# Kernel tuning notes

Measured on AMD Instinct MI355X. Metric: run time of the kernel, lower is better.

The kernel has to match this reference:

```python
import jax, jax.numpy as jnp
import numpy as np

N_NODES = 50000
N_EDGES = 800000
DIM = 64
N_HEADS = 4


def setup_inputs() -> dict:
    key = jax.random.key(0)
    ks = jax.random.split(key, 7)
    x = jax.random.normal(ks[0], (N_NODES, DIM), dtype=jnp.float32)
    Wq = jax.random.normal(ks[1], (DIM, DIM), dtype=jnp.float32) / np.sqrt(DIM)
    Wk = jax.random.normal(ks[2], (DIM, DIM), dtype=jnp.float32) / np.sqrt(DIM)
    Wv = jax.random.normal(ks[3], (DIM, DIM), dtype=jnp.float32) / np.sqrt(DIM)
    Wo = jax.random.normal(ks[4], (DIM, DIM), dtype=jnp.float32) / np.sqrt(DIM)
    src = jax.random.randint(ks[5], (N_EDGES,), 0, N_NODES, dtype=jnp.int32)
    dst = jax.random.randint(ks[6], (N_EDGES,), 0, N_NODES, dtype=jnp.int32)
    return {"x": x, "Wq": Wq, "Wk": Wk, "Wv": Wv, "Wo": Wo, "src": src, "dst": dst}


def _scatter_softmax(scores, dst, n_nodes):
    # scores: [E, H]; per-destination-node softmax over incoming edges.
    m = jax.ops.segment_max(scores, dst, num_segments=n_nodes)  # [N, H]
    m = jnp.maximum(m, jnp.float32(-1e9))  # mirror the -1e9 init of the torch code
    ex = jnp.exp(scores - m[dst])  # [E, H]
    denom = jax.ops.segment_sum(ex, dst, num_segments=n_nodes)  # [N, H]
    return ex / (denom[dst] + 1e-9)


def reference(x, Wq, Wk, Wv, Wo, src, dst):
    N, D = x.shape
    H = N_HEADS
    Dh = D // H
    q = (x @ Wq).reshape(N, H, Dh)
    k = (x @ Wk).reshape(N, H, Dh)
    v = (x @ Wv).reshape(N, H, Dh)
    # per-edge attention logits: [E, H]
    scores = jnp.einsum("ehd,ehd->eh", q[dst], k[src]) / jnp.sqrt(jnp.float32(Dh))
    alpha = _scatter_softmax(scores, dst, N)  # [E, H]
    # weighted aggregation of source values onto destination nodes
    agg = jax.ops.segment_sum(alpha[:, :, None] * v[src], dst, num_segments=N)  # [N, H, Dh]
    return agg.reshape(N, D) @ Wo
```

## Files before the change

### kernel.cpp

```cpp
#include <hip/hip_runtime.h>
#include <math.h>

#define HEADS 4
#define DH 16
#define D 64
#define MAXDEG 64
#define NXCD 8

typedef unsigned short ushort_t;
typedef unsigned int uint_t;

__device__ __forceinline__ float bf2f(ushort_t u) {
    return __uint_as_float(((uint_t)u) << 16);
}
__device__ __forceinline__ ushort_t f2bf(float f) {
    uint_t u = __float_as_uint(f);
    u = (u + 0x7FFFu + ((u >> 16) & 1u)) >> 16;
    return (ushort_t)u;
}
__device__ __forceinline__ float bflo(uint_t u) { return __uint_as_float(u << 16); }
__device__ __forceinline__ float bfhi(uint_t u) { return __uint_as_float(u & 0xFFFF0000u); }
__device__ __forceinline__ uint_t pack2(float a, float b) {
    return (uint_t)f2bf(a) | ((uint_t)f2bf(b) << 16);
}

__global__ __launch_bounds__(256) void qkv_kernel(const float* __restrict__ x,
                                                  const float* __restrict__ Wq,
                                                  const float* __restrict__ Wk,
                                                  const float* __restrict__ Wv,
                                                  ushort_t* __restrict__ qbf,
                                                  ushort_t* __restrict__ kbf,
                                                  ushort_t* __restrict__ vbf,
                                                  int* __restrict__ cursor,
                                                  int N) {
    __shared__ float wq[D][D];
    __shared__ float wk[D][D];
    __shared__ float wv[D][D];
    __shared__ float xs[16][D];

    int tid = threadIdx.x;
    for (int i = tid; i < D * D; i += 256) {
        wq[i >> 6][i & 63] = Wq[i];
        wk[i >> 6][i & 63] = Wk[i];
        wv[i >> 6][i & 63] = Wv[i];
    }

    int c = tid & 63;
    int g = tid >> 6;
    int row = tid >> 4;
    int col4 = tid & 15;

    int ntiles = (N + 15) >> 4;
    for (int tile = blockIdx.x; tile < ntiles; tile += gridDim.x) {
        int n0t = tile * 16;
        __syncthreads();
        float4 xv = make_float4(0.f, 0.f, 0.f, 0.f);
        if (n0t + row < N) xv = *(const float4*)(x + (size_t)(n0t + row) * D + col4 * 4);
        *(float4*)&xs[row][col4 * 4] = xv;
        __syncthreads();

        float aq0=0,aq1=0,aq2=0,aq3=0, ak0=0,ak1=0,ak2=0,ak3=0, av0=0,av1=0,av2=0,av3=0;
#pragma unroll 8
        for (int d = 0; d < D; ++d) {
            float wqv = wq[d][c], wkv = wk[d][c], wvv = wv[d][c];
            float x0 = xs[g*4+0][d], x1 = xs[g*4+1][d], x2 = xs[g*4+2][d], x3 = xs[g*4+3][d];
            aq0 += x0*wqv; ak0 += x0*wkv; av0 += x0*wvv;
            aq1 += x1*wqv; ak1 += x1*wkv; av1 += x1*wvv;
            aq2 += x2*wqv; ak2 += x2*wkv; av2 += x2*wvv;
            aq3 += x3*wqv; ak3 += x3*wkv; av3 += x3*wvv;
        }
        int nb = n0t + g * 4;
        if (nb+0 < N) { qbf[(size_t)(nb+0)*D+c]=f2bf(aq0); kbf[(size_t)(nb+0)*D+c]=f2bf(ak0); vbf[(size_t)(nb+0)*D+c]=f2bf(av0); }
        if (nb+1 < N) { qbf[(size_t)(nb+1)*D+c]=f2bf(aq1); kbf[(size_t)(nb+1)*D+c]=f2bf(ak1); vbf[(size_t)(nb+1)*D+c]=f2bf(av1); }
        if (nb+2 < N) { qbf[(size_t)(nb+2)*D+c]=f2bf(aq2); kbf[(size_t)(nb+2)*D+c]=f2bf(ak2); vbf[(size_t)(nb+2)*D+c]=f2bf(av2); }
        if (nb+3 < N) { qbf[(size_t)(nb+3)*D+c]=f2bf(aq3); kbf[(size_t)(nb+3)*D+c]=f2bf(ak3); vbf[(size_t)(nb+3)*D+c]=f2bf(av3); }
    }

    for (int i = blockIdx.x * 256 + tid; i < N; i += gridDim.x * 256) cursor[i] = 0;
}

__global__ __launch_bounds__(256) void scatter_kernel(const int* __restrict__ src,
                                                      const int* __restrict__ dst,
                                                      int* __restrict__ cursor,
                                                      ushort_t* __restrict__ csr,
                                                      int E, int N) {
    int p      = blockIdx.x & (NXCD - 1);
    int chunk  = blockIdx.x >> 3;
    int nchunk = gridDim.x >> 3;
    int lo = (int)((long long)N * p / NXCD);
    int hi = (int)((long long)N * (p + 1) / NXCD);
    int e0 = (int)((long long)E * chunk / nchunk);
    int e1 = (int)((long long)E * (chunk + 1) / nchunk);

    for (int e = e0 + threadIdx.x; e < e1; e += 256) {
        int d = dst[e];
        if (d >= lo && d < hi) {
            int pos = atomicAdd(&cursor[d], 1);
            if (pos < MAXDEG) csr[(size_t)d * MAXDEG + pos] = (ushort_t)src[e];
        }
    }
}

__global__ __launch_bounds__(256) void attn_kernel(const ushort_t* __restrict__ qbf,
                                                   const ushort_t* __restrict__ kbf,
                                                   const ushort_t* __restrict__ vbf,
                                                   const ushort_t* __restrict__ csr,
                                                   const int* __restrict__ cursor,
                                                   ushort_t* __restrict__ aggbf,
                                                   int N) {
    int lane = threadIdx.x & 63;
    int wave = threadIdx.x >> 6;
    int node = blockIdx.x * 4 + wave;
    if (node >= N) return;

    int hp  = lane & 3;
    int el  = lane >> 2;
    int hd  = (lane & 31) >> 3;
    int par = lane >> 5;
    int dp2 = 2 * (lane & 31);

    int cnt = cursor[node]; if (cnt > MAXDEG) cnt = MAXDEG;
    const ushort_t* row = csr + (size_t)node * MAXDEG;

    float qr[16];
    {
        const uint4* qp = (const uint4*)(qbf + (size_t)node * D + hp * DH);
        uint4 qa = qp[0], qb = qp[1];
        qr[0]=bflo(qa.x);  qr[1]=bfhi(qa.x);  qr[2]=bflo(qa.y);  qr[3]=bfhi(qa.y);
        qr[4]=bflo(qa.z);  qr[5]=bfhi(qa.z);  qr[6]=bflo(qa.w);  qr[7]=bfhi(qa.w);
        qr[8]=bflo(qb.x);  qr[9]=bfhi(qb.x);  qr[10]=bflo(qb.y); qr[11]=bfhi(qb.y);
        qr[12]=bflo(qb.z); qr[13]=bfhi(qb.z); qr[14]=bflo(qb.w); qr[15]=bfhi(qb.w);
    }

    int s0=0, s1=0, s2=0, s3=0;
    float sc0=-1e30f, sc1=-1e30f, sc2=-1e30f, sc3=-1e30f;

#define PH1SB(sb, sv, scv)                                                      \
    if ((sb) * 16 < cnt) {                                                      \
        int eidx = (sb) * 16 + el;                                              \
        if (eidx < cnt) sv = row[eidx];                                         \
        const uint4* kp = (const uint4*)(kbf + (size_t)sv * D + hp * DH);       \
        uint4 ka = kp[0], kb = kp[1];                                           \
        float dot =                                                             \
          bflo(ka.x)*qr[0]  + bfhi(ka.x)*qr[1]                                  \
        + bflo(ka.y)*qr[2]  + bfhi(ka.y)*qr[3]                                  \
        + bflo(ka.z)*qr[4]  + bfhi(ka.z)*qr[5]                                  \
        + bflo(ka.w)*qr[6]  + bfhi(ka.w)*qr[7]                                  \
        + bflo(kb.x)*qr[8]  + bfhi(kb.x)*qr[9]                                  \
        + bflo(kb.y)*qr[10] + bfhi(kb.y)*qr[11]                                 \
        + bflo(kb.z)*qr[12] + bfhi(kb.z)*qr[13]                                 \
        + bflo(kb.w)*qr[14] + bfhi(kb.w)*qr[15];                                \
        scv = (eidx < cnt) ? dot * 0.25f : -1e30f;                              \
    }
    PH1SB(0, s0, sc0)
    PH1SB(1, s1, sc1)
    PH1SB(2, s2, sc2)
    PH1SB(3, s3, sc3)
#undef PH1SB

    float mloc = fmaxf(fmaxf(sc0, sc1), fmaxf(sc2, sc3));
    mloc = fmaxf(mloc, __shfl_xor(mloc, 4, 64));
    mloc = fmaxf(mloc, __shfl_xor(mloc, 8, 64));
    mloc = fmaxf(mloc, __shfl_xor(mloc, 16, 64));
    mloc = fmaxf(mloc, __shfl_xor(mloc, 32, 64));
    mloc = fmaxf(mloc, -1e9f);

    float pv0 = __expf(sc0 - mloc);
    float pv1 = __expf(sc1 - mloc);
    float pv2 = __expf(sc2 - mloc);
    float pv3 = __expf(sc3 - mloc);
    float ls = (pv0 + pv1) + (pv2 + pv3);
    ls += __shfl_xor(ls, 4, 64);
    ls += __shfl_xor(ls, 8, 64);
    ls += __shfl_xor(ls, 16, 64);
    ls += __shfl_xor(ls, 32, 64);

    float inv = 1.f / (__shfl(ls, hd, 64) + 1e-9f);

    float2 a0 = {0.f, 0.f}, a1 = {0.f, 0.f};
#define PH3SB(sb, sv, pvv)                                                      \
    if ((sb) * 16 < cnt) {                                                      \
        int lim = cnt - (sb) * 16; if (lim > 16) lim = 16;                      \
        for (int e2 = 0; e2 < lim; e2 += 4) {                                   \
            int L0 = 4 * (e2 + par);                                            \
            int ss0 = __shfl(sv, L0, 64);                                       \
            float p0 = __shfl(pvv, L0 + hd, 64);                                \
            uint_t w0 = *(const uint_t*)(vbf + (size_t)ss0 * D + dp2);          \
            a0.x += p0 * bflo(w0);                                              \
            a0.y += p0 * bfhi(w0);                                              \
            int L1 = 4 * (e2 + 2 + par);                                        \
            int ss1 = __shfl(sv, L1, 64);                                       \
            float p1 = __shfl(pvv, L1 + hd, 64);                                \
            uint_t w1 = *(const uint_t*)(vbf + (size_t)ss1 * D + dp2);          \
            a1.x += p1 * bflo(w1);                                              \
            a1.y += p1 * bfhi(w1);                                              \
        }                                                                       \
    }
    PH3SB(0, s0, pv0)
    PH3SB(1, s1, pv1)
    PH3SB(2, s2, pv2)
    PH3SB(3, s3, pv3)
#undef PH3SB

    float ax = a0.x + a1.x, ay = a0.y + a1.y;
    ax += __shfl_xor(ax, 32, 64);
    ay += __shfl_xor(ay, 32, 64);
    if (lane < 32) {
        *(uint_t*)(aggbf + (size_t)node * D + dp2) = pack2(ax * inv, ay * inv);
    }
}

__global__ __launch_bounds__(256) void out_kernel(const ushort_t* __restrict__ aggbf,
                                                  const float* __restrict__ Wo,
                                                  float* __restrict__ out, int N) {
    __shared__ float wo[D][D];
    __shared__ float xs[16][D];

    int tid = threadIdx.x;
    for (int i = tid; i < D * D; i += 256) wo[i >> 6][i & 63] = Wo[i];

    int c = tid & 63;
    int g = tid >> 6;
    int row = tid >> 4;
    int col4 = tid & 15;

    int ntiles = (N + 15) >> 4;
    for (int tile = blockIdx.x; tile < ntiles; tile += gridDim.x) {
        int n0 = tile * 16;
        __syncthreads();
        uint2 av = make_uint2(0u, 0u);
        if (n0 + row < N) av = *(const uint2*)(aggbf + (size_t)(n0 + row) * D + col4 * 4);
        xs[row][col4 * 4 + 0] = bflo(av.x);
        xs[row][col4 * 4 + 1] = bfhi(av.x);
        xs[row][col4 * 4 + 2] = bflo(av.y);
        xs[row][col4 * 4 + 3] = bfhi(av.y);
        __syncthreads();

        float a0 = 0.f, a1 = 0.f, a2 = 0.f, a3 = 0.f;
#pragma unroll 8
        for (int d = 0; d < D; ++d) {
            float w = wo[d][c];
            a0 += xs[g*4+0][d] * w;
            a1 += xs[g*4+1][d] * w;
            a2 += xs[g*4+2][d] * w;
            a3 += xs[g*4+3][d] * w;
        }
        int nb = n0 + g * 4;
        if (nb+0 < N) out[(size_t)(nb+0)*D+c] = a0;
        if (nb+1 < N) out[(size_t)(nb+1)*D+c] = a1;
        if (nb+2 < N) out[(size_t)(nb+2)*D+c] = a2;
        if (nb+3 < N) out[(size_t)(nb+3)*D+c] = a3;
    }
}

extern "C" void kernel_launch(void* const* d_in, const int* in_sizes, int n_in,
                              void* d_out, int out_size, void* d_ws, size_t ws_size,
                              hipStream_t stream) {
    const float* x  = (const float*)d_in[0];
    const float* Wq = (const float*)d_in[1];
    const float* Wk = (const float*)d_in[2];
    const float* Wv = (const float*)d_in[3];
    const float* Wo = (const float*)d_in[4];
    const int* src  = (const int*)d_in[5];
    const int* dst  = (const int*)d_in[6];
    float* out = (float*)d_out;

    int N = in_sizes[0] / D;
    int E = in_sizes[5];

    char* ws = (char*)d_ws;
    ushort_t* qbf   = (ushort_t*)ws;  ws += (size_t)N * D * 2;
    ushort_t* kbf   = (ushort_t*)ws;  ws += (size_t)N * D * 2;
    ushort_t* vbf   = (ushort_t*)ws;  ws += (size_t)N * D * 2;
    ushort_t* aggbf = (ushort_t*)ws;  ws += (size_t)N * D * 2;
    int* cursor     = (int*)ws;       ws += (size_t)N * 4;
    ushort_t* csr   = (ushort_t*)ws;  ws += (size_t)N * MAXDEG * 2;

    int nTiles16 = (N + 15) / 16;
    int gemmGrid = nTiles16 < 2048 ? nTiles16 : 2048;
    int attnGrid = (N + 3) / 4;

    qkv_kernel<<<gemmGrid, 256, 0, stream>>>(x, Wq, Wk, Wv, qbf, kbf, vbf, cursor, N);
    scatter_kernel<<<2048, 256, 0, stream>>>(src, dst, cursor, csr, E, N);
    attn_kernel<<<attnGrid, 256, 0, stream>>>(qbf, kbf, vbf, csr, cursor, aggbf, N);
    out_kernel<<<gemmGrid, 256, 0, stream>>>(aggbf, Wo, out, N);
}
```

Baseline: 129.2 us.

## Scatter edges in one pass with vectorized loads and packed atomicOr CSR writes

The old scatter kernel made each of 8 XCD partitions re-read every edge and keep only destinations in its node range. It is replaced by a single pass where each thread loads 4 edges with int4 loads and inserts the source index into a 32-bit packed CSR word using atomicOr. This needs the CSR buffer zeroed beforehand, so a hipMemsetAsync now clears both the cursor and the CSR region, replacing the cursor zeroing in the qkv kernel. The cost is one extra memset pass over about 6.6 MB and an atomic per CSR write, in exchange for reading the edge arrays only once. The per-XCD locality of the cursor atomics is also lost.

```diff
diff --git a/kernel.cpp b/kernel.cpp
--- a/kernel.cpp
+++ b/kernel.cpp
@@ -31,7 +31,6 @@
                                                   ushort_t* __restrict__ qbf,
                                                   ushort_t* __restrict__ kbf,
                                                   ushort_t* __restrict__ vbf,
-                                                  int* __restrict__ cursor,
                                                   int N) {
     __shared__ float wq[D][D];
     __shared__ float wk[D][D];
@@ -75,28 +74,31 @@
         if (nb+2 < N) { qbf[(size_t)(nb+2)*D+c]=f2bf(aq2); kbf[(size_t)(nb+2)*D+c]=f2bf(ak2); vbf[(size_t)(nb+2)*D+c]=f2bf(av2); }
         if (nb+3 < N) { qbf[(size_t)(nb+3)*D+c]=f2bf(aq3); kbf[(size_t)(nb+3)*D+c]=f2bf(ak3); vbf[(size_t)(nb+3)*D+c]=f2bf(av3); }
     }
-
-    for (int i = blockIdx.x * 256 + tid; i < N; i += gridDim.x * 256) cursor[i] = 0;
 }
 
 __global__ __launch_bounds__(256) void scatter_kernel(const int* __restrict__ src,
                                                       const int* __restrict__ dst,
                                                       int* __restrict__ cursor,
-                                                      ushort_t* __restrict__ csr,
-                                                      int E, int N) {
-    int p      = blockIdx.x & (NXCD - 1);
-    int chunk  = blockIdx.x >> 3;
-    int nchunk = gridDim.x >> 3;
-    int lo = (int)((long long)N * p / NXCD);
-    int hi = (int)((long long)N * (p + 1) / NXCD);
-    int e0 = (int)((long long)E * chunk / nchunk);
-    int e1 = (int)((long long)E * (chunk + 1) / nchunk);
-
-    for (int e = e0 + threadIdx.x; e < e1; e += 256) {
-        int d = dst[e];
-        if (d >= lo && d < hi) {
-            int pos = atomicAdd(&cursor[d], 1);
-            if (pos < MAXDEG) csr[(size_t)d * MAXDEG + pos] = (ushort_t)src[e];
+                                                      uint_t* __restrict__ csr32,
+                                                      int E) {
+    int e0 = (blockIdx.x * 256 + threadIdx.x) * 4;
+    if (e0 + 3 < E) {
+        int4 s4 = *(const int4*)(src + e0);
+        int4 d4 = *(const int4*)(dst + e0);
+        int p;
+        p = atomicAdd(&cursor[d4.x], 1);
+        if (p < MAXDEG) atomicOr(&csr32[d4.x * (MAXDEG/2) + (p >> 1)], ((uint_t)s4.x) << ((p & 1) * 16));
+        p = atomicAdd(&cursor[d4.y], 1);
+        if (p < MAXDEG) atomicOr(&csr32[d4.y * (MAXDEG/2) + (p >> 1)], ((uint_t)s4.y) << ((p & 1) * 16));
+        p = atomicAdd(&cursor[d4.z], 1);
+        if (p < MAXDEG) atomicOr(&csr32[d4.z * (MAXDEG/2) + (p >> 1)], ((uint_t)s4.z) << ((p & 1) * 16));
+        p = atomicAdd(&cursor[d4.w], 1);
+        if (p < MAXDEG) atomicOr(&csr32[d4.w * (MAXDEG/2) + (p >> 1)], ((uint_t)s4.w) << ((p & 1) * 16));
+    } else {
+        for (int e = e0; e < E; ++e) {
+            int d = dst[e];
+            int p = atomicAdd(&cursor[d], 1);
+            if (p < MAXDEG) atomicOr(&csr32[d * (MAXDEG/2) + (p >> 1)], ((uint_t)src[e]) << ((p & 1) * 16));
         }
     }
 }
@@ -278,10 +280,12 @@
 
     int nTiles16 = (N + 15) / 16;
     int gemmGrid = nTiles16 < 2048 ? nTiles16 : 2048;
+    int scatGrid = ((E + 3) / 4 + 255) / 256;
     int attnGrid = (N + 3) / 4;
 
-    qkv_kernel<<<gemmGrid, 256, 0, stream>>>(x, Wq, Wk, Wv, qbf, kbf, vbf, cursor, N);
-    scatter_kernel<<<2048, 256, 0, stream>>>(src, dst, cursor, csr, E, N);
+    hipMemsetAsync(cursor, 0, (size_t)N * 4 + (size_t)N * MAXDEG * 2, stream);
+    qkv_kernel<<<gemmGrid, 256, 0, stream>>>(x, Wq, Wk, Wv, qbf, kbf, vbf, N);
+    scatter_kernel<<<scatGrid, 256, 0, stream>>>(src, dst, cursor, (uint_t*)csr, E);
     attn_kernel<<<attnGrid, 256, 0, stream>>>(qbf, kbf, vbf, csr, cursor, aggbf, N);
     out_kernel<<<gemmGrid, 256, 0, stream>>>(aggbf, Wo, out, N);
 }
```

New measurement: 177.0 us. 1.37x slower.
